# Kernel tuning notes

Hardware: AMD Instinct MI355X
Metric: run time of the kernel (lower is better)

The kernel has to match this reference:

```python
import jax, jax.numpy as jnp
import numpy as np

N, D = 6144, 128
NUM_CLASSES, NUM_BATCHES = 20, 5
MIN_T, MAX_T = 0.1, 1.0
TEMP_BATCH = 0.5  # fixed per-batch-key temperature set in __init__
EPS = 1e-8        # F.cosine_similarity eps


def _class_weights(labels, n):
    c = jnp.bincount(labels, length=n).astype(jnp.float32)
    w = 1.0 / c
    return w / w.sum()


def setup_inputs() -> dict:
    key = jax.random.key(0)
    k1, k2, k3 = jax.random.split(key, 3)
    x = jax.random.normal(k1, (N, D), dtype=jnp.float32)
    targets = jax.random.randint(k2, (N,), 0, NUM_CLASSES)
    batch0 = jax.random.randint(k3, (N,), 0, NUM_BATCHES)
    return {
        "input": x,
        "temperature": jnp.float32(0.25),
        "weight_target": _class_weights(targets, NUM_CLASSES),
        "weight_batch0": _class_weights(batch0, NUM_BATCHES),
        "targets": targets,
        "batch0": batch0,
    }


def _snn_losses(S, pos_mask, neg_mask):
    # S: [N,N] exp-similarities; masks include/exclude self consistently with torch code
    diag = jnp.diagonal(S)
    pos_sum = jnp.einsum('ij,ij->i', S, pos_mask.astype(S.dtype)) - diag  # self is in pos_mask
    neg_sum = jnp.einsum('ij,ij->i', S, neg_mask.astype(S.dtype))
    cnt_pos = pos_mask.sum(axis=1)  # includes self
    cnt_neg = neg_mask.sum(axis=1)
    valid = (cnt_pos >= 2) & (cnt_neg >= 1)
    pos_safe = jnp.where(valid, pos_sum, 1.0)
    neg_safe = jnp.where(valid, neg_sum, 1.0)
    loss_i = -jnp.log(pos_safe / (pos_safe + neg_safe))
    return loss_i, valid


def _weighted_class_sum(loss_i, valid, labels, weights, num_segments):
    lsum = jax.ops.segment_sum(jnp.where(valid, loss_i, 0.0), labels, num_segments=num_segments)
    cnt = jax.ops.segment_sum(valid.astype(jnp.float32), labels, num_segments=num_segments)
    mean = lsum / jnp.maximum(cnt, 1.0)
    return jnp.sum(jnp.where(cnt > 0, mean * weights, 0.0))


def reference(input, temperature, weight_target, weight_batch0, targets, batch0):
    t = jnp.clip(temperature, MIN_T, MAX_T)
    norms = jnp.maximum(jnp.linalg.norm(input, axis=1, keepdims=True), EPS)
    xn = input / norms
    sim = xn @ xn.T  # [N, N] cosine similarity

    same_t = targets[:, None] == targets[None, :]

    # ----- target (cell-type) SNN loss -----
    S_t = jnp.exp(sim / t)
    loss_i, valid = _snn_losses(S_t, same_t, ~same_t)
    loss_target = _weighted_class_sum(loss_i, valid, targets, weight_target, NUM_CLASSES)

    # ----- batch-effect loss (one batch key), reciprocal of -log -----
    S_b = jnp.exp(sim / TEMP_BATCH)
    same_b = batch0[:, None] == batch0[None, :]
    pos_mask = same_t & same_b
    neg_mask = same_t & (~same_b)
    loss_bi, valid_b = _snn_losses(S_b, pos_mask, neg_mask)
    loss_bi = jnp.where(valid_b, 1.0 / jnp.where(valid_b, loss_bi, 1.0), 0.0)
    loss_batch = _weighted_class_sum(loss_bi, valid_b, batch0, weight_batch0, NUM_BATCHES)
    # single batch key -> mean over batch keys is just loss_batch

    return 0.9 * loss_target + 0.1 * loss_batch
```

## Files before the change

### kernel.cpp

```cpp
#include <hip/hip_runtime.h>
#include <hip/hip_bf16.h>
#include <math.h>

#define NN 6144
#define DD 128
#define NCLS 20
#define NBATCH 5
#define NB 48
#define NPAIR (NB * (NB + 1) / 2)

typedef float f32x4 __attribute__((ext_vector_type(4)));
typedef short bf16x8 __attribute__((ext_vector_type(8)));

#define SOFF (NN * DD / 2)
#define HOFF (SOFF + 4 * NN)
#define AOFF (HOFF + 120)

__global__ __launch_bounds__(1024) void k_zero(const int* __restrict__ tg,
                                               const int* __restrict__ bt,
                                               float* __restrict__ ws) {
    const int t = threadIdx.x;
    if (blockIdx.x > 0) {
        ws[SOFF + (blockIdx.x - 1) * 1024 + t] = 0.0f;
        return;
    }
    __shared__ int h[NCLS + NCLS * NBATCH];
    if (t < NCLS + NCLS * NBATCH) h[t] = 0;
    if (t < 50) ws[AOFF + t] = 0.0f;
    __syncthreads();
    for (int i = t; i < NN; i += 1024) {
        int c = tg[i], b = bt[i];
        atomicAdd(&h[c], 1);
        atomicAdd(&h[NCLS + c * NBATCH + b], 1);
    }
    __syncthreads();
    int* hp = (int*)(ws + HOFF);
    if (t < NCLS + NCLS * NBATCH) hp[t] = h[t];
}

__global__ __launch_bounds__(256) void k_prep(const float* __restrict__ x,
                                              float* __restrict__ ws) {
    const int t = threadIdx.x;
    const int lane = t & 63;
    const int row = blockIdx.x * 4 + (t >> 6);
    float2 v = *(const float2*)(x + row * DD + 2 * lane);
    float s = v.x * v.x + v.y * v.y;
#pragma unroll
    for (int m = 1; m < 64; m <<= 1) s += __shfl_xor(s, m, 64);
    float rinv = 1.0f / fmaxf(sqrtf(s), 1e-8f);
    __hip_bfloat16 h0 = __float2bfloat16(v.x * rinv);
    __hip_bfloat16 h1 = __float2bfloat16(v.y * rinv);
    ushort2 u;
    u.x = *(ushort*)&h0;
    u.y = *(ushort*)&h1;
    ushort* xnb = (ushort*)ws;
    *(ushort2*)(xnb + row * DD + 2 * lane) = u;
}

__global__ __launch_bounds__(256) void k_main(const float* __restrict__ temp,
                                              const int* __restrict__ tg,
                                              const int* __restrict__ bt,
                                              float* __restrict__ ws) {
    __shared__ ushort tA[128][72];
    __shared__ ushort tB[128][72];
    __shared__ int tgA[128], btA[128], tgB[128], btB[128];
    __shared__ float sStat[4][256];

    const ushort* xnb = (const ushort*)ws;
    float* PT = ws + SOFF;
    float* TT = PT + NN;
    float* PB = PT + 2 * NN;
    float* TB = PT + 3 * NN;

    int bi = 0, rem = blockIdx.x;
    while (rem >= NB - bi) { rem -= NB - bi; ++bi; }
    const int bj = bi + rem;
    const int I = bi * 128, J = bj * 128;
    const bool isDiag = (bi == bj);

    const int t = threadIdx.x;
    const int w = t >> 6;
    const int lane = t & 63;
    const int tx16 = lane & 15;
    const int quad = lane >> 4;
    const int rowBase = (w >> 1) * 64;
    const int colBase = (w & 1) * 64;

    const float tc = fminf(fmaxf(temp[0], 0.1f), 1.0f);
    const float c1 = 1.4426950408889634f / tc;
    const float c2 = 2.8853900817779268f;

    if (t < 128) { tgA[t] = tg[I + t]; btA[t] = bt[I + t]; }
    else { int u = t - 128; tgB[u] = tg[J + u]; btB[u] = bt[J + u]; }
#pragma unroll
    for (int s = 0; s < 4; ++s) sStat[s][t] = 0.0f;

    f32x4 acc[4][4];
#pragma unroll
    for (int mt = 0; mt < 4; ++mt)
#pragma unroll
        for (int nt = 0; nt < 4; ++nt) acc[mt][nt] = (f32x4){0.f, 0.f, 0.f, 0.f};

    for (int kc = 0; kc < 2; ++kc) {
        if (kc) __syncthreads();
        {
            const int r0 = t >> 3, ch = t & 7;
            const ushort* gA = xnb + (I + r0) * DD + kc * 64 + ch * 8;
            const ushort* gB = xnb + (J + r0) * DD + kc * 64 + ch * 8;
#pragma unroll
            for (int it = 0; it < 4; ++it) {
                *(float4*)&tA[r0 + 32 * it][ch * 8] = *(const float4*)(gA + 32 * it * DD);
                *(float4*)&tB[r0 + 32 * it][ch * 8] = *(const float4*)(gB + 32 * it * DD);
            }
        }
        __syncthreads();
#pragma unroll
        for (int ks = 0; ks < 2; ++ks) {
            bf16x8 a[4], b[4];
            const int ko = ks * 32 + quad * 8;
#pragma unroll
            for (int mt = 0; mt < 4; ++mt)
                a[mt] = *(const bf16x8*)&tA[rowBase + 16 * mt + tx16][ko];
#pragma unroll
            for (int nt = 0; nt < 4; ++nt)
                b[nt] = *(const bf16x8*)&tB[colBase + 16 * nt + tx16][ko];
#pragma unroll
            for (int mt = 0; mt < 4; ++mt)
#pragma unroll
                for (int nt = 0; nt < 4; ++nt)
                    acc[mt][nt] = __builtin_amdgcn_mfma_f32_16x16x32_bf16(
                        a[mt], b[nt], acc[mt][nt], 0, 0, 0);
        }
    }

    float cPT[4] = {0}, cTT[4] = {0}, cPB[4] = {0}, cTB[4] = {0};
    int tjv[4], bjv[4];
#pragma unroll
    for (int nt = 0; nt < 4; ++nt) {
        int jl = colBase + 16 * nt + tx16;
        tjv[nt] = tgB[jl];
        bjv[nt] = btB[jl];
    }

#pragma unroll
    for (int mt = 0; mt < 4; ++mt) {
        float rPT[4] = {0}, rTT[4] = {0}, rPB[4] = {0}, rTB[4] = {0};
        int til[4], bil[4];
#pragma unroll
        for (int p = 0; p < 4; ++p) {
            int il = rowBase + 16 * mt + 4 * quad + p;
            til[p] = tgA[il];
            bil[p] = btA[il];
        }
#pragma unroll
        for (int nt = 0; nt < 4; ++nt) {
            const int jl = colBase + 16 * nt + tx16;
#pragma unroll
            for (int p = 0; p < 4; ++p) {
                const int il = rowBase + 16 * mt + 4 * quad + p;
                float s = acc[mt][nt][p];
                float et = __builtin_amdgcn_exp2f(c1 * s);
                float eb = __builtin_amdgcn_exp2f(c2 * s);
                bool nd = !isDiag || (il != jl);
                bool st = (til[p] == tjv[nt]) && nd;
                bool sb = (bil[p] == bjv[nt]);
                rTT[p] += nd ? et : 0.f;
                rPT[p] += st ? et : 0.f;
                rTB[p] += st ? eb : 0.f;
                rPB[p] += (st && sb) ? eb : 0.f;
                if (!isDiag) {
                    cTT[nt] += et;
                    cPT[nt] += st ? et : 0.f;
                    cTB[nt] += st ? eb : 0.f;
                    cPB[nt] += (st && sb) ? eb : 0.f;
                }
            }
        }
#pragma unroll
        for (int p = 0; p < 4; ++p) {
            float vPT = rPT[p], vTT = rTT[p], vPB = rPB[p], vTB = rTB[p];
#pragma unroll
            for (int m = 1; m < 16; m <<= 1) {
                vPT += __shfl_xor(vPT, m, 64);
                vTT += __shfl_xor(vTT, m, 64);
                vPB += __shfl_xor(vPB, m, 64);
                vTB += __shfl_xor(vTB, m, 64);
            }
            if (tx16 == 0) {
                int il = rowBase + 16 * mt + 4 * quad + p;
                atomicAdd(&sStat[0][il], vPT);
                atomicAdd(&sStat[1][il], vTT);
                atomicAdd(&sStat[2][il], vPB);
                atomicAdd(&sStat[3][il], vTB);
            }
        }
    }
    if (!isDiag) {
#pragma unroll
        for (int nt = 0; nt < 4; ++nt) {
            float vPT = cPT[nt], vTT = cTT[nt], vPB = cPB[nt], vTB = cTB[nt];
#pragma unroll
            for (int m = 16; m < 64; m <<= 1) {
                vPT += __shfl_xor(vPT, m, 64);
                vTT += __shfl_xor(vTT, m, 64);
                vPB += __shfl_xor(vPB, m, 64);
                vTB += __shfl_xor(vTB, m, 64);
            }
            if (quad == 0) {
                int cl = 128 + colBase + 16 * nt + tx16;
                atomicAdd(&sStat[0][cl], vPT);
                atomicAdd(&sStat[1][cl], vTT);
                atomicAdd(&sStat[2][cl], vPB);
                atomicAdd(&sStat[3][cl], vTB);
            }
        }
    }

    __syncthreads();
    if (t < 128) {
        int gi = I + t;
        atomicAdd(&PT[gi], sStat[0][t]);
        atomicAdd(&TT[gi], sStat[1][t]);
        atomicAdd(&PB[gi], sStat[2][t]);
        atomicAdd(&TB[gi], sStat[3][t]);
    } else if (!isDiag) {
        int gj = J + (t - 128);
        atomicAdd(&PT[gj], sStat[0][t]);
        atomicAdd(&TT[gj], sStat[1][t]);
        atomicAdd(&PB[gj], sStat[2][t]);
        atomicAdd(&TB[gj], sStat[3][t]);
    }
}

__global__ __launch_bounds__(256) void k_fin(const int* __restrict__ tg,
                                             const int* __restrict__ bt,
                                             float* __restrict__ ws) {
    __shared__ float ls_t[NCLS], ct_t[NCLS], ls_b[NBATCH], cb_b[NBATCH];
    const int t = threadIdx.x;
    if (t < NCLS) { ls_t[t] = 0.f; ct_t[t] = 0.f; }
    if (t < NBATCH) { ls_b[t] = 0.f; cb_b[t] = 0.f; }
    __syncthreads();
    const float* PT = ws + SOFF;
    const float* TT = PT + NN;
    const float* PB = PT + 2 * NN;
    const float* TB = PT + 3 * NN;
    const int* hp = (const int*)(ws + HOFF);
    const int i = blockIdx.x * 256 + t;
    float pt = PT[i], tt = TT[i], pb = PB[i], tb = TB[i];
    int ti = tg[i], bi = bt[i];
    int cp = hp[ti];
    int cpb = hp[NCLS + ti * NBATCH + bi];
    if (cp >= 2 && (NN - cp) >= 1) {
        float loss = -logf(pt / (pt + (tt - pt)));
        atomicAdd(&ls_t[ti], loss);
        atomicAdd(&ct_t[ti], 1.f);
    }
    if (cpb >= 2 && (cp - cpb) >= 1) {
        float lb = -logf(pb / (pb + (tb - pb)));
        atomicAdd(&ls_b[bi], 1.f / lb);
        atomicAdd(&cb_b[bi], 1.f);
    }
    __syncthreads();
    float* acc = ws + AOFF;
    if (t < NCLS) {
        if (ls_t[t] != 0.f) atomicAdd(&acc[t], ls_t[t]);
        if (ct_t[t] != 0.f) atomicAdd(&acc[NCLS + t], ct_t[t]);
    }
    if (t < NBATCH) {
        if (ls_b[t] != 0.f) atomicAdd(&acc[2 * NCLS + t], ls_b[t]);
        if (cb_b[t] != 0.f) atomicAdd(&acc[2 * NCLS + NBATCH + t], cb_b[t]);
    }
}

__global__ void k_out(const float* __restrict__ wt, const float* __restrict__ wb,
                      const float* __restrict__ ws, float* __restrict__ out) {
    if (threadIdx.x == 0 && blockIdx.x == 0) {
        const float* acc = ws + AOFF;
        float lt = 0.f, lb = 0.f;
        for (int c = 0; c < NCLS; ++c)
            if (acc[NCLS + c] > 0.f) lt += (acc[c] / acc[NCLS + c]) * wt[c];
        for (int b = 0; b < NBATCH; ++b)
            if (acc[2 * NCLS + NBATCH + b] > 0.f)
                lb += (acc[2 * NCLS + b] / acc[2 * NCLS + NBATCH + b]) * wb[b];
        out[0] = 0.9f * lt + 0.1f * lb;
    }
}

extern "C" void kernel_launch(void* const* d_in, const int* in_sizes, int n_in,
                              void* d_out, int out_size, void* d_ws, size_t ws_size,
                              hipStream_t stream) {
    const float* x    = (const float*)d_in[0];
    const float* temp = (const float*)d_in[1];
    const float* wt   = (const float*)d_in[2];
    const float* wb   = (const float*)d_in[3];
    const int*   tg   = (const int*)d_in[4];
    const int*   bt   = (const int*)d_in[5];
    float* out = (float*)d_out;
    float* ws = (float*)d_ws;

    k_zero<<<25, 1024, 0, stream>>>(tg, bt, ws);
    k_prep<<<NN / 4, 256, 0, stream>>>(x, ws);
    k_main<<<NPAIR, 256, 0, stream>>>(temp, tg, bt, ws);
    k_fin<<<NN / 256, 256, 0, stream>>>(tg, bt, ws);
    k_out<<<1, 64, 0, stream>>>(wt, wb, ws, out);
}
```

Measured before the change: 123.1 us.

## Fuse zeroing into prep, merge finish kernels, use transpose-style shuffle reductions

Drops the separate zeroing kernel by having the first prep blocks clear the stat buffers, and folds the histogram, per-row loss and final weighting into one single-block finish kernel, cutting launches from five to three. The per-row and per-column shuffle reductions in the main kernel now use a butterfly transpose-reduce, so each lane ends up owning one output and fewer shuffles are issued. The cost is that the finish step runs on only one block, so that tail is serialized.

```diff
diff --git a/kernel.cpp b/kernel.cpp
--- a/kernel.cpp
+++ b/kernel.cpp
@@ -13,34 +13,14 @@
 typedef short bf16x8 __attribute__((ext_vector_type(8)));
 
 #define SOFF (NN * DD / 2)
-#define HOFF (SOFF + 4 * NN)
-#define AOFF (HOFF + 120)
-
-__global__ __launch_bounds__(1024) void k_zero(const int* __restrict__ tg,
-                                               const int* __restrict__ bt,
-                                               float* __restrict__ ws) {
-    const int t = threadIdx.x;
-    if (blockIdx.x > 0) {
-        ws[SOFF + (blockIdx.x - 1) * 1024 + t] = 0.0f;
-        return;
-    }
-    __shared__ int h[NCLS + NCLS * NBATCH];
-    if (t < NCLS + NCLS * NBATCH) h[t] = 0;
-    if (t < 50) ws[AOFF + t] = 0.0f;
-    __syncthreads();
-    for (int i = t; i < NN; i += 1024) {
-        int c = tg[i], b = bt[i];
-        atomicAdd(&h[c], 1);
-        atomicAdd(&h[NCLS + c * NBATCH + b], 1);
-    }
-    __syncthreads();
-    int* hp = (int*)(ws + HOFF);
-    if (t < NCLS + NCLS * NBATCH) hp[t] = h[t];
-}
 
 __global__ __launch_bounds__(256) void k_prep(const float* __restrict__ x,
                                               float* __restrict__ ws) {
     const int t = threadIdx.x;
+    if (blockIdx.x < 24) {
+        float4 z = {0.f, 0.f, 0.f, 0.f};
+        *(float4*)(ws + SOFF + blockIdx.x * 1024 + t * 4) = z;
+    }
     const int lane = t & 63;
     const int row = blockIdx.x * 4 + (t >> 6);
     float2 v = *(const float2*)(x + row * DD + 2 * lane);
@@ -91,7 +71,7 @@
     const float c2 = 2.8853900817779268f;
 
     if (t < 128) { tgA[t] = tg[I + t]; btA[t] = bt[I + t]; }
-    else { int u = t - 128; tgB[u] = tg[J + u]; btB[u] = bt[J + u]; }
+    else { int u2 = t - 128; tgB[u2] = tg[J + u2]; btB[u2] = bt[J + u2]; }
 #pragma unroll
     for (int s = 0; s < 4; ++s) sStat[s][t] = 0.0f;
 
@@ -141,6 +121,9 @@
         tjv[nt] = tgB[jl];
         bjv[nt] = btB[jl];
     }
+    const bool up3 = (tx16 >> 3) & 1;
+    const bool up2 = (tx16 >> 2) & 1;
+    const int pOwn = tx16 >> 2;
 
 #pragma unroll
     for (int mt = 0; mt < 4; ++mt) {
@@ -176,44 +159,60 @@
                 }
             }
         }
-#pragma unroll
-        for (int p = 0; p < 4; ++p) {
-            float vPT = rPT[p], vTT = rTT[p], vPB = rPB[p], vTB = rTB[p];
-#pragma unroll
-            for (int m = 1; m < 16; m <<= 1) {
-                vPT += __shfl_xor(vPT, m, 64);
-                vTT += __shfl_xor(vTT, m, 64);
-                vPB += __shfl_xor(vPB, m, 64);
-                vTB += __shfl_xor(vTB, m, 64);
-            }
-            if (tx16 == 0) {
-                int il = rowBase + 16 * mt + 4 * quad + p;
-                atomicAdd(&sStat[0][il], vPT);
-                atomicAdd(&sStat[1][il], vTT);
-                atomicAdd(&sStat[2][il], vPB);
-                atomicAdd(&sStat[3][il], vTB);
-            }
+        float res[4];
+        float* arr[4] = {rPT, rTT, rPB, rTB};
+#pragma unroll
+        for (int s = 0; s < 4; ++s) {
+            float* v = arr[s];
+#pragma unroll
+            for (int i = 0; i < 2; ++i) {
+                float send = up3 ? v[i] : v[i + 2];
+                float keep = up3 ? v[i + 2] : v[i];
+                v[i] = keep + __shfl_xor(send, 8, 64);
+            }
+            {
+                float send = up2 ? v[0] : v[1];
+                float keep = up2 ? v[1] : v[0];
+                v[0] = keep + __shfl_xor(send, 4, 64);
+            }
+            v[0] += __shfl_xor(v[0], 2, 64);
+            v[0] += __shfl_xor(v[0], 1, 64);
+            res[s] = v[0];
+        }
+        if ((tx16 & 3) == 0) {
+            int il = rowBase + 16 * mt + 4 * quad + pOwn;
+            atomicAdd(&sStat[0][il], res[0]);
+            atomicAdd(&sStat[1][il], res[1]);
+            atomicAdd(&sStat[2][il], res[2]);
+            atomicAdd(&sStat[3][il], res[3]);
         }
     }
     if (!isDiag) {
-#pragma unroll
-        for (int nt = 0; nt < 4; ++nt) {
-            float vPT = cPT[nt], vTT = cTT[nt], vPB = cPB[nt], vTB = cTB[nt];
-#pragma unroll
-            for (int m = 16; m < 64; m <<= 1) {
-                vPT += __shfl_xor(vPT, m, 64);
-                vTT += __shfl_xor(vTT, m, 64);
-                vPB += __shfl_xor(vPB, m, 64);
-                vTB += __shfl_xor(vTB, m, 64);
-            }
-            if (quad == 0) {
-                int cl = 128 + colBase + 16 * nt + tx16;
-                atomicAdd(&sStat[0][cl], vPT);
-                atomicAdd(&sStat[1][cl], vTT);
-                atomicAdd(&sStat[2][cl], vPB);
-                atomicAdd(&sStat[3][cl], vTB);
-            }
-        }
+        const bool q1 = (quad >> 1) & 1;
+        const bool q0 = quad & 1;
+        float resc[4];
+        float* arrc[4] = {cPT, cTT, cPB, cTB};
+#pragma unroll
+        for (int s = 0; s < 4; ++s) {
+            float* v = arrc[s];
+#pragma unroll
+            for (int i = 0; i < 2; ++i) {
+                float send = q1 ? v[i] : v[i + 2];
+                float keep = q1 ? v[i + 2] : v[i];
+                v[i] = keep + __shfl_xor(send, 32, 64);
+            }
+            {
+                float send = q0 ? v[0] : v[1];
+                float keep = q0 ? v[1] : v[0];
+                v[0] = keep + __shfl_xor(send, 16, 64);
+            }
+            resc[s] = v[0];
+        }
+        int cl = 128 + colBase + 16 * quad + tx16;
+        atomicAdd(&sStat[0][cl], resc[0]);
+        atomicAdd(&sStat[1][cl], resc[1]);
+        atomicAdd(&sStat[2][cl], resc[2]);
+        atomicAdd(&sStat[3][cl], resc[3]);
     }
 
     __syncthreads();
@@ -232,56 +231,59 @@
     }
 }
 
-__global__ __launch_bounds__(256) void k_fin(const int* __restrict__ tg,
-                                             const int* __restrict__ bt,
-                                             float* __restrict__ ws) {
-    __shared__ float ls_t[NCLS], ct_t[NCLS], ls_b[NBATCH], cb_b[NBATCH];
+__global__ __launch_bounds__(1024) void k_fin(const int* __restrict__ tg,
+                                              const int* __restrict__ bt,
+                                              const float* __restrict__ wt,
+                                              const float* __restrict__ wb,
+                                              const float* __restrict__ ws,
+                                              float* __restrict__ out) {
+    __shared__ int hh[NCLS + NCLS * NBATCH];
+    __shared__ float ph[16][52];
     const int t = threadIdx.x;
-    if (t < NCLS) { ls_t[t] = 0.f; ct_t[t] = 0.f; }
-    if (t < NBATCH) { ls_b[t] = 0.f; cb_b[t] = 0.f; }
+    const int wv = t >> 6;
+    if (t < NCLS + NCLS * NBATCH) hh[t] = 0;
+    for (int i = t; i < 16 * 52; i += 1024) ((float*)ph)[i] = 0.0f;
+    __syncthreads();
+    for (int i = t; i < NN; i += 1024) {
+        int c = tg[i], b = bt[i];
+        atomicAdd(&hh[c], 1);
+        atomicAdd(&hh[NCLS + c * NBATCH + b], 1);
+    }
     __syncthreads();
     const float* PT = ws + SOFF;
     const float* TT = PT + NN;
     const float* PB = PT + 2 * NN;
     const float* TB = PT + 3 * NN;
-    const int* hp = (const int*)(ws + HOFF);
-    const int i = blockIdx.x * 256 + t;
-    float pt = PT[i], tt = TT[i], pb = PB[i], tb = TB[i];
-    int ti = tg[i], bi = bt[i];
-    int cp = hp[ti];
-    int cpb = hp[NCLS + ti * NBATCH + bi];
-    if (cp >= 2 && (NN - cp) >= 1) {
-        float loss = -logf(pt / (pt + (tt - pt)));
-        atomicAdd(&ls_t[ti], loss);
-        atomicAdd(&ct_t[ti], 1.f);
-    }
-    if (cpb >= 2 && (cp - cpb) >= 1) {
-        float lb = -logf(pb / (pb + (tb - pb)));
-        atomicAdd(&ls_b[bi], 1.f / lb);
-        atomicAdd(&cb_b[bi], 1.f);
-    }
-    __syncthreads();
-    float* acc = ws + AOFF;
-    if (t < NCLS) {
-        if (ls_t[t] != 0.f) atomicAdd(&acc[t], ls_t[t]);
-        if (ct_t[t] != 0.f) atomicAdd(&acc[NCLS + t], ct_t[t]);
-    }
-    if (t < NBATCH) {
-        if (ls_b[t] != 0.f) atomicAdd(&acc[2 * NCLS + t], ls_b[t]);
-        if (cb_b[t] != 0.f) atomicAdd(&acc[2 * NCLS + NBATCH + t], cb_b[t]);
-    }
-}
-
-__global__ void k_out(const float* __restrict__ wt, const float* __restrict__ wb,
-                      const float* __restrict__ ws, float* __restrict__ out) {
-    if (threadIdx.x == 0 && blockIdx.x == 0) {
-        const float* acc = ws + AOFF;
+    for (int i = t; i < NN; i += 1024) {
+        float pt = PT[i], tt = TT[i], pb = PB[i], tb = TB[i];
+        int ti = tg[i], bi = bt[i];
+        int cp = hh[ti];
+        int cpb = hh[NCLS + ti * NBATCH + bi];
+        if (cp >= 2 && (NN - cp) >= 1) {
+            float loss = logf(tt) - logf(pt);
+            atomicAdd(&ph[wv][ti], loss);
+            atomicAdd(&ph[wv][20 + ti], 1.0f);
+        }
+        if (cpb >= 2 && (cp - cpb) >= 1) {
+            float lb = logf(tb) - logf(pb);
+            atomicAdd(&ph[wv][40 + bi], 1.0f / lb);
+            atomicAdd(&ph[wv][45 + bi], 1.0f);
+        }
+    }
+    __syncthreads();
+    if (t < 50) {
+        float s = 0.f;
+#pragma unroll
+        for (int w2 = 0; w2 < 16; ++w2) s += ph[w2][t];
+        ph[0][t] = s;
+    }
+    __syncthreads();
+    if (t == 0) {
         float lt = 0.f, lb = 0.f;
         for (int c = 0; c < NCLS; ++c)
-            if (acc[NCLS + c] > 0.f) lt += (acc[c] / acc[NCLS + c]) * wt[c];
+            if (ph[0][20 + c] > 0.f) lt += (ph[0][c] / ph[0][20 + c]) * wt[c];
         for (int b = 0; b < NBATCH; ++b)
-            if (acc[2 * NCLS + NBATCH + b] > 0.f)
-                lb += (acc[2 * NCLS + b] / acc[2 * NCLS + NBATCH + b]) * wb[b];
+            if (ph[0][45 + b] > 0.f) lb += (ph[0][40 + b] / ph[0][45 + b]) * wb[b];
         out[0] = 0.9f * lt + 0.1f * lb;
     }
 }
@@ -298,9 +300,7 @@
     float* out = (float*)d_out;
     float* ws = (float*)d_ws;
 
-    k_zero<<<25, 1024, 0, stream>>>(tg, bt, ws);
     k_prep<<<NN / 4, 256, 0, stream>>>(x, ws);
     k_main<<<NPAIR, 256, 0, stream>>>(temp, tg, bt, ws);
-    k_fin<<<NN / 256, 256, 0, stream>>>(tg, bt, ws);
-    k_out<<<1, 64, 0, stream>>>(wt, wb, ws, out);
+    k_fin<<<1, 1024, 0, stream>>>(tg, bt, wt, wb, ws, out);
 }
```

Result: slower. 155.7 us (+26.5%).
